# Performance work log

Measured on AMD Instinct MI355X. Metric: run time of the kernel, lower is better.

Reference implementation:

```python
import jax, jax.numpy as jnp
import numpy as np

N_NODES = 50000


def setup_inputs() -> dict:
    key = jax.random.key(0)
    k1, k2, k3, k4 = jax.random.split(key, 4)
    x = jax.random.normal(k1, (N_NODES, 128), dtype=jnp.float32)
    edge_index = jax.random.randint(k2, (2, 800000), 0, N_NODES, dtype=jnp.int64)
    W = jax.random.normal(k3, (128, 128), dtype=jnp.float32) * 0.05
    b = jax.random.normal(k4, (128,), dtype=jnp.float32) * 0.05
    return {"x": x, "edge_index": edge_index, "W": W, "b": b}


def reference(x, edge_index, W, b):
    # x: [N, C_in], edge_index: [2, E]
    row, col = edge_index[0], edge_index[1]
    n = x.shape[0]
    # degree of each node as a source (bincount over row)
    deg = jax.ops.segment_sum(jnp.ones_like(row, dtype=x.dtype), row, num_segments=n)
    # deg^{-1/2} with inf -> 0 (deg == 0 case)
    deg_inv_sqrt = jnp.where(deg > 0, jax.lax.rsqrt(jnp.maximum(deg, 1.0)) * jnp.where(deg > 0, 1.0, 0.0), 0.0)
    deg_inv_sqrt = jnp.where(deg > 0, deg ** -0.5, 0.0)
    norm = deg_inv_sqrt[row] * deg_inv_sqrt[col]  # [E]
    # gather, scale, scatter-add: agg[row] += x[col] * norm
    msgs = x[col] * norm[:, None]  # [E, C_in]
    agg = jax.ops.segment_sum(msgs, row, num_segments=n)  # [N, C_in]
    # linear
    return agg @ W.T + b
```

## Files before the change

kernel.cpp:

```cpp
#include <hip/hip_runtime.h>
#include <hip/hip_bf16.h>


typedef short v8s __attribute__((ext_vector_type(8)));
typedef float v4f __attribute__((ext_vector_type(4)));

#define ELLCAP 64
#define NSHARD 16
#define SUBCAP 384
#define ROWSTRIDE 136

static __device__ __forceinline__ unsigned int f2bf(float f) {
    __hip_bfloat16 h = __float2bfloat16(f);
    return (unsigned int)__builtin_bit_cast(unsigned short, h);
}

__global__ __launch_bounds__(256) void k_bin(
    const int* __restrict__ idx, int* __restrict__ gbin,
    unsigned int* __restrict__ pairs, const float4* __restrict__ w4,
    ushort4* __restrict__ wb4, const float2* __restrict__ x2,
    unsigned int* __restrict__ xs32, int E, int ncast, int N, int nbins) {
    int b = blockIdx.x;
    const int t = threadIdx.x;
    if (b < 16) {
        int i = b * 256 + t;
        float4 v = w4[i];
        ushort4 o;
        o.x = (unsigned short)f2bf(v.x);
        o.y = (unsigned short)f2bf(v.y);
        o.z = (unsigned short)f2bf(v.z);
        o.w = (unsigned short)f2bf(v.w);
        wb4[i] = o;
        return;
    }
    b -= 16;
    if (b < ncast) {
        int base = b * 4096;
#pragma unroll 4
        for (int it = 0; it < 16; ++it) {
            int i = base + it * 256 + t;
            int lr = i >> 6;
            unsigned ov = 0u;
            if (lr < N) {
                float2 v = x2[i];
                ov = f2bf(v.x) | (f2bf(v.y) << 16);
            }
            xs32[i] = ov;
        }
        return;
    }
    b -= ncast;
    __shared__ int hist[256];
    __shared__ int hist2[256];
    __shared__ int base[256];
    hist[t] = 0;
    hist2[t] = 0;
    __syncthreads();

    int e0 = b * 2048 + t * 8;
    int nv = E - e0;
    nv = nv > 8 ? 8 : (nv < 0 ? 0 : nv);
    int rows[8], cols[8];
    if (nv == 8) {
        int4 a0 = *(const int4*)&idx[e0];
        int4 a1 = *(const int4*)&idx[e0 + 4];
        int4 c0 = *(const int4*)&idx[E + e0];
        int4 c1 = *(const int4*)&idx[E + e0 + 4];
        rows[0] = a0.x; rows[1] = a0.y; rows[2] = a0.z; rows[3] = a0.w;
        rows[4] = a1.x; rows[5] = a1.y; rows[6] = a1.z; rows[7] = a1.w;
        cols[0] = c0.x; cols[1] = c0.y; cols[2] = c0.z; cols[3] = c0.w;
        cols[4] = c1.x; cols[5] = c1.y; cols[6] = c1.z; cols[7] = c1.w;
    } else {
        for (int k = 0; k < 8; ++k) {
            rows[k] = (k < nv) ? idx[e0 + k] : 0;
            cols[k] = (k < nv) ? idx[E + e0 + k] : 0;
        }
    }
#pragma unroll
    for (int k = 0; k < 8; ++k)
        if (k < nv) atomicAdd(&hist[rows[k] >> 8], 1);
    __syncthreads();
    const int shard = b & (NSHARD - 1);
    if (t < nbins)
        base[t] = atomicAdd(&gbin[t * NSHARD + shard], hist[t]);
    __syncthreads();
#pragma unroll
    for (int k = 0; k < 8; ++k) {
        if (k < nv) {
            int bin = rows[k] >> 8;
            int pos = base[bin] + atomicAdd(&hist2[bin], 1);
            if (pos < SUBCAP)
                pairs[((size_t)bin * NSHARD + shard) * SUBCAP + pos] =
                    (unsigned)(((rows[k] & 255) << 16) | cols[k]);
        }
    }
}

__global__ __launch_bounds__(1024) void k_deg(
    const unsigned int* __restrict__ pairs, const int* __restrict__ gbin,
    float* __restrict__ dis, int N) {
    __shared__ int cnt[256];
    __shared__ int scnt[NSHARD];
    const int bin = blockIdx.x;
    const int t = threadIdx.x;
    if (t < 256) cnt[t] = 0;
    if (t < NSHARD) {
        int m = gbin[bin * NSHARD + t];
        scnt[t] = m > SUBCAP ? SUBCAP : m;
    }
    __syncthreads();
    for (int s = 0; s < NSHARD; ++s) {
        int ms = scnt[s];
        size_t pb = ((size_t)bin * NSHARD + s) * SUBCAP;
        for (int i = t; i < ms; i += 1024)
            atomicAdd(&cnt[pairs[pb + i] >> 16], 1);
    }
    __syncthreads();
    if (t < 256) {
        int r = bin * 256 + t;
        int d = cnt[t];
        dis[r] = (r < N && d > 0) ? rsqrtf((float)d) : 0.f;
    }
}

__global__ __launch_bounds__(512) void k_fused(
    const unsigned int* __restrict__ pairs, const int* __restrict__ gbin,
    const float* __restrict__ dis, const unsigned int* __restrict__ xs32,
    const v8s* __restrict__ Wb8, const float* __restrict__ bias,
    float* __restrict__ out, int N) {
    __shared__ __align__(16) unsigned short lell[64 * ELLCAP];
    __shared__ int cnt[64];
    __shared__ int scnt[NSHARD];
    __shared__ __align__(16) unsigned short smem[64 * ROWSTRIDE];
    const int bin = blockIdx.x >> 2, sub = blockIdx.x & 3;
    const int t = threadIdx.x;
    if (t < 64) cnt[t] = 0;
    if (t < NSHARD) {
        int m = gbin[bin * NSHARD + t];
        scnt[t] = m > SUBCAP ? SUBCAP : m;
    }
    __syncthreads();
    for (int s = 0; s < NSHARD; ++s) {
        int ms = scnt[s];
        size_t pb = ((size_t)bin * NSHARD + s) * SUBCAP;
        for (int i = t; i < ms; i += 512) {
            unsigned pv = pairs[pb + i];
            int lr = pv >> 16;
            if ((lr >> 6) == sub) {
                int slot = atomicAdd(&cnt[lr & 63], 1);
                if (slot < ELLCAP)
                    lell[(lr & 63) * ELLCAP + slot] = (unsigned short)(pv & 0xFFFF);
            }
        }
    }
    __syncthreads();

    const int wv = t >> 6, lane = t & 63;
    const int r0 = bin * 256 + sub * 64;
    for (int i = 0; i < 8; ++i) {
        int lrow = wv * 8 + i;
        int n = r0 + lrow;
        float acc0 = 0.f, acc1 = 0.f;
        if (n < N) {
            int dtrue = cnt[lrow];
            int d = dtrue > ELLCAP ? ELLCAP : dtrue;
            int cl = lell[lrow * ELLCAP + lane];
            int c = (lane < d) ? cl : N;
            float dcf = dis[c];
            int dcb = __builtin_bit_cast(int, dcf);
            for (int j = 0; j < d; j += 16) {
                int cc[16];
#pragma unroll
                for (int u = 0; u < 16; ++u)
                    cc[u] = __builtin_amdgcn_readlane(c, j + u);
                unsigned uu[16];
#pragma unroll
                for (int u = 0; u < 16; ++u)
                    uu[u] = xs32[(size_t)cc[u] * 64 + lane];
                float sc[16];
#pragma unroll
                for (int u = 0; u < 16; ++u)
                    sc[u] = __builtin_bit_cast(
                        float, __builtin_amdgcn_readlane(dcb, j + u));
#pragma unroll
                for (int u = 0; u < 16; ++u) {
                    acc0 = fmaf(sc[u], __builtin_bit_cast(float, uu[u] << 16), acc0);
                    acc1 = fmaf(sc[u],
                                __builtin_bit_cast(float, uu[u] & 0xFFFF0000u), acc1);
                }
            }
            float s = (dtrue > 0) ? rsqrtf((float)dtrue) : 0.f;
            acc0 *= s;
            acc1 *= s;
        }
        unsigned pack = f2bf(acc0) | (f2bf(acc1) << 16);
        *(unsigned int*)&smem[(size_t)lrow * ROWSTRIDE + lane * 2] = pack;
    }
    __syncthreads();

    {
        int g = wv >> 2, w4 = wv & 3;
        int quad = lane >> 4, m16 = lane & 15;
        int lrow = g * 32 + (w4 & 1) * 16 + m16;
        v8s afrag[4];
#pragma unroll
        for (int kk = 0; kk < 4; ++kk)
            afrag[kk] = *(const v8s*)&smem[lrow * ROWSTRIDE + kk * 32 + quad * 8];
        int rbase = r0 + g * 32 + (w4 & 1) * 16 + quad * 4;
        int jbase = (w4 >> 1) * 64;
#pragma unroll
        for (int jt = 0; jt < 4; ++jt) {
            int jcol = jbase + jt * 16 + m16;
            v4f acc = {0.f, 0.f, 0.f, 0.f};
#pragma unroll
            for (int kk = 0; kk < 4; ++kk) {
                v8s bfrag = Wb8[jcol * 16 + kk * 4 + quad];
                acc = __builtin_amdgcn_mfma_f32_16x16x32_bf16(afrag[kk], bfrag,
                                                              acc, 0, 0, 0);
            }
            float bj = bias[jcol];
#pragma unroll
            for (int r = 0; r < 4; ++r) {
                int row = rbase + r;
                if (row < N) out[(size_t)row * 128 + jcol] = acc[r] + bj;
            }
        }
    }
}

extern "C" void kernel_launch(void* const* d_in, const int* in_sizes, int n_in,
                              void* d_out, int out_size, void* d_ws, size_t ws_size,
                              hipStream_t stream) {
    const float* x = (const float*)d_in[0];
    const int* idx = (const int*)d_in[1];
    const float* W = (const float*)d_in[2];
    const float* b = (const float*)d_in[3];
    float* out = (float*)d_out;

    const int N = in_sizes[0] / 128;
    const int E = in_sizes[1] / 2;
    const int nbins = (N + 255) / 256;
    const int nrows = nbins * 256;
    const int ncast = nbins * 4;

    char* p = (char*)d_ws;
    auto alloc = [&](size_t bytes) {
        char* r = p;
        p += (bytes + 63) & ~(size_t)63;
        return r;
    };
    int* gbin = (int*)alloc((size_t)nbins * NSHARD * 4);
    unsigned int* pairs =
        (unsigned int*)alloc((size_t)nbins * NSHARD * SUBCAP * 4);
    float* dis = (float*)alloc((size_t)nrows * 4);
    unsigned int* xs = (unsigned int*)alloc((size_t)nrows * 128 * 2);
    ushort4* wb = (ushort4*)alloc(128 * 128 * 2);

    hipMemsetAsync(gbin, 0, (size_t)nbins * NSHARD * sizeof(int), stream);

    const int bblocks = 16 + ncast + (E + 2047) / 2048;
    k_bin<<<bblocks, 256, 0, stream>>>(idx, gbin, pairs, (const float4*)W, wb,
                                       (const float2*)x, xs, E, ncast, N, nbins);
    k_deg<<<nbins, 1024, 0, stream>>>(pairs, gbin, dis, N);
    k_fused<<<nbins * 4, 512, 0, stream>>>(pairs, gbin, dis, xs, (const v8s*)wb,
                                           b, out, N);
}
```

Before: 158.7 us.

## Count degrees with global atomics in binning, shrink fused grid to 128-row blocks

Degree counting moves into the binning kernel as global atomics on a per-node counter array. The shared-memory k_deg pass is replaced by a trivial elementwise rsqrt kernel. The fused kernel now handles 128 rows per block instead of 64, cutting redundant rescans of each bin's pair list from four to two, and it gathers 32 neighbours per unrolled batch. The trade-offs are 800k global atomics in k_bin, roughly double the LDS per block (lower occupancy), and higher register pressure from the wider gather.

```diff
diff --git a/kernel.cpp b/kernel.cpp
--- a/kernel.cpp
+++ b/kernel.cpp
@@ -16,7 +16,7 @@
 }
 
 __global__ __launch_bounds__(256) void k_bin(
-    const int* __restrict__ idx, int* __restrict__ gbin,
+    const int* __restrict__ idx, int* __restrict__ gbin, int* __restrict__ deg,
     unsigned int* __restrict__ pairs, const float4* __restrict__ w4,
     ushort4* __restrict__ wb4, const float2* __restrict__ x2,
     unsigned int* __restrict__ xs32, int E, int ncast, int N, int nbins) {
@@ -77,8 +77,12 @@
         }
     }
 #pragma unroll
-    for (int k = 0; k < 8; ++k)
-        if (k < nv) atomicAdd(&hist[rows[k] >> 8], 1);
+    for (int k = 0; k < 8; ++k) {
+        if (k < nv) {
+            atomicAdd(&hist[rows[k] >> 8], 1);
+            atomicAdd(&deg[rows[k]], 1);
+        }
+    }
     __syncthreads();
     const int shard = b & (NSHARD - 1);
     if (t < nbins)
@@ -96,31 +100,17 @@
     }
 }
 
-__global__ __launch_bounds__(1024) void k_deg(
-    const unsigned int* __restrict__ pairs, const int* __restrict__ gbin,
-    float* __restrict__ dis, int N) {
-    __shared__ int cnt[256];
-    __shared__ int scnt[NSHARD];
-    const int bin = blockIdx.x;
-    const int t = threadIdx.x;
-    if (t < 256) cnt[t] = 0;
-    if (t < NSHARD) {
-        int m = gbin[bin * NSHARD + t];
-        scnt[t] = m > SUBCAP ? SUBCAP : m;
-    }
-    __syncthreads();
-    for (int s = 0; s < NSHARD; ++s) {
-        int ms = scnt[s];
-        size_t pb = ((size_t)bin * NSHARD + s) * SUBCAP;
-        for (int i = t; i < ms; i += 1024)
-            atomicAdd(&cnt[pairs[pb + i] >> 16], 1);
-    }
-    __syncthreads();
-    if (t < 256) {
-        int r = bin * 256 + t;
-        int d = cnt[t];
-        dis[r] = (r < N && d > 0) ? rsqrtf((float)d) : 0.f;
-    }
+__global__ __launch_bounds__(256) void k_dis(const int* __restrict__ deg,
+                                             float* __restrict__ dis, int N,
+                                             int nrows) {
+    int r = blockIdx.x * 256 + threadIdx.x;
+    if (r >= nrows) return;
+    float v = 0.f;
+    if (r < N) {
+        int d = deg[r];
+        if (d > 0) v = rsqrtf((float)d);
+    }
+    dis[r] = v;
 }
 
 __global__ __launch_bounds__(512) void k_fused(
@@ -128,13 +118,13 @@
     const float* __restrict__ dis, const unsigned int* __restrict__ xs32,
     const v8s* __restrict__ Wb8, const float* __restrict__ bias,
     float* __restrict__ out, int N) {
-    __shared__ __align__(16) unsigned short lell[64 * ELLCAP];
-    __shared__ int cnt[64];
+    __shared__ __align__(16) unsigned short lell[128 * ELLCAP];
+    __shared__ int cnt[128];
     __shared__ int scnt[NSHARD];
-    __shared__ __align__(16) unsigned short smem[64 * ROWSTRIDE];
-    const int bin = blockIdx.x >> 2, sub = blockIdx.x & 3;
+    __shared__ __align__(16) unsigned short smem[128 * ROWSTRIDE];
+    const int bin = blockIdx.x >> 1, sub = blockIdx.x & 1;
     const int t = threadIdx.x;
-    if (t < 64) cnt[t] = 0;
+    if (t < 128) cnt[t] = 0;
     if (t < NSHARD) {
         int m = gbin[bin * NSHARD + t];
         scnt[t] = m > SUBCAP ? SUBCAP : m;
@@ -146,19 +136,20 @@
         for (int i = t; i < ms; i += 512) {
             unsigned pv = pairs[pb + i];
             int lr = pv >> 16;
-            if ((lr >> 6) == sub) {
-                int slot = atomicAdd(&cnt[lr & 63], 1);
+            if ((lr >> 7) == sub) {
+                int la = lr & 127;
+                int slot = atomicAdd(&cnt[la], 1);
                 if (slot < ELLCAP)
-                    lell[(lr & 63) * ELLCAP + slot] = (unsigned short)(pv & 0xFFFF);
+                    lell[la * ELLCAP + slot] = (unsigned short)(pv & 0xFFFF);
             }
         }
     }
     __syncthreads();
 
     const int wv = t >> 6, lane = t & 63;
-    const int r0 = bin * 256 + sub * 64;
-    for (int i = 0; i < 8; ++i) {
-        int lrow = wv * 8 + i;
+    const int r0 = bin * 256 + sub * 128;
+    for (int i = 0; i < 16; ++i) {
+        int lrow = wv * 16 + i;
         int n = r0 + lrow;
         float acc0 = 0.f, acc1 = 0.f;
         if (n < N) {
@@ -168,28 +159,28 @@
             int c = (lane < d) ? cl : N;
             float dcf = dis[c];
             int dcb = __builtin_bit_cast(int, dcf);
-            for (int j = 0; j < d; j += 16) {
-                int cc[16];
-#pragma unroll
-                for (int u = 0; u < 16; ++u)
+            for (int j = 0; j < d; j += 32) {
+                int cc[32];
+#pragma unroll
+                for (int u = 0; u < 32; ++u)
                     cc[u] = __builtin_amdgcn_readlane(c, j + u);
-                unsigned uu[16];
-#pragma unroll
-                for (int u = 0; u < 16; ++u)
+                unsigned uu[32];
+#pragma unroll
+                for (int u = 0; u < 32; ++u)
                     uu[u] = xs32[(size_t)cc[u] * 64 + lane];
-                float sc[16];
-#pragma unroll
-                for (int u = 0; u < 16; ++u)
+                float sc[32];
+#pragma unroll
+                for (int u = 0; u < 32; ++u)
                     sc[u] = __builtin_bit_cast(
                         float, __builtin_amdgcn_readlane(dcb, j + u));
 #pragma unroll
-                for (int u = 0; u < 16; ++u) {
+                for (int u = 0; u < 32; ++u) {
                     acc0 = fmaf(sc[u], __builtin_bit_cast(float, uu[u] << 16), acc0);
                     acc1 = fmaf(sc[u],
                                 __builtin_bit_cast(float, uu[u] & 0xFFFF0000u), acc1);
                 }
             }
-            float s = (dtrue > 0) ? rsqrtf((float)dtrue) : 0.f;
+            float s = dis[n];
             acc0 *= s;
             acc1 *= s;
         }
@@ -201,28 +192,31 @@
     {
         int g = wv >> 2, w4 = wv & 3;
         int quad = lane >> 4, m16 = lane & 15;
-        int lrow = g * 32 + (w4 & 1) * 16 + m16;
-        v8s afrag[4];
-#pragma unroll
-        for (int kk = 0; kk < 4; ++kk)
-            afrag[kk] = *(const v8s*)&smem[lrow * ROWSTRIDE + kk * 32 + quad * 8];
-        int rbase = r0 + g * 32 + (w4 & 1) * 16 + quad * 4;
-        int jbase = (w4 >> 1) * 64;
-#pragma unroll
-        for (int jt = 0; jt < 4; ++jt) {
-            int jcol = jbase + jt * 16 + m16;
-            v4f acc = {0.f, 0.f, 0.f, 0.f};
-#pragma unroll
-            for (int kk = 0; kk < 4; ++kk) {
-                v8s bfrag = Wb8[jcol * 16 + kk * 4 + quad];
-                acc = __builtin_amdgcn_mfma_f32_16x16x32_bf16(afrag[kk], bfrag,
-                                                              acc, 0, 0, 0);
-            }
-            float bj = bias[jcol];
-#pragma unroll
-            for (int r = 0; r < 4; ++r) {
-                int row = rbase + r;
-                if (row < N) out[(size_t)row * 128 + jcol] = acc[r] + bj;
+#pragma unroll
+        for (int rg = 0; rg < 2; ++rg) {
+            int lrow = rg * 64 + g * 32 + (w4 & 1) * 16 + m16;
+            v8s afrag[4];
+#pragma unroll
+            for (int kk = 0; kk < 4; ++kk)
+                afrag[kk] = *(const v8s*)&smem[lrow * ROWSTRIDE + kk * 32 + quad * 8];
+            int rbase = r0 + rg * 64 + g * 32 + (w4 & 1) * 16 + quad * 4;
+            int jbase = (w4 >> 1) * 64;
+#pragma unroll
+            for (int jt = 0; jt < 4; ++jt) {
+                int jcol = jbase + jt * 16 + m16;
+                v4f acc = {0.f, 0.f, 0.f, 0.f};
+#pragma unroll
+                for (int kk = 0; kk < 4; ++kk) {
+                    v8s bfrag = Wb8[jcol * 16 + kk * 4 + quad];
+                    acc = __builtin_amdgcn_mfma_f32_16x16x32_bf16(afrag[kk], bfrag,
+                                                                  acc, 0, 0, 0);
+                }
+                float bj = bias[jcol];
+#pragma unroll
+                for (int r = 0; r < 4; ++r) {
+                    int row = rbase + r;
+                    if (row < N) out[(size_t)row * 128 + jcol] = acc[r] + bj;
+                }
             }
         }
     }
@@ -249,19 +243,21 @@
         p += (bytes + 63) & ~(size_t)63;
         return r;
     };
-    int* gbin = (int*)alloc((size_t)nbins * NSHARD * 4);
+    int* deg = (int*)alloc((size_t)nrows * 4 + (size_t)nbins * NSHARD * 4);
+    int* gbin = deg + nrows;
     unsigned int* pairs =
         (unsigned int*)alloc((size_t)nbins * NSHARD * SUBCAP * 4);
     float* dis = (float*)alloc((size_t)nrows * 4);
     unsigned int* xs = (unsigned int*)alloc((size_t)nrows * 128 * 2);
     ushort4* wb = (ushort4*)alloc(128 * 128 * 2);
 
-    hipMemsetAsync(gbin, 0, (size_t)nbins * NSHARD * sizeof(int), stream);
+    hipMemsetAsync(deg, 0, ((size_t)nrows + (size_t)nbins * NSHARD) * 4, stream);
 
     const int bblocks = 16 + ncast + (E + 2047) / 2048;
-    k_bin<<<bblocks, 256, 0, stream>>>(idx, gbin, pairs, (const float4*)W, wb,
-                                       (const float2*)x, xs, E, ncast, N, nbins);
-    k_deg<<<nbins, 1024, 0, stream>>>(pairs, gbin, dis, N);
-    k_fused<<<nbins * 4, 512, 0, stream>>>(pairs, gbin, dis, xs, (const v8s*)wb,
+    k_bin<<<bblocks, 256, 0, stream>>>(idx, gbin, deg, pairs, (const float4*)W,
+                                       wb, (const float2*)x, xs, E, ncast, N,
+                                       nbins);
+    k_dis<<<nrows / 256, 256, 0, stream>>>(deg, dis, N, nrows);
+    k_fused<<<nbins * 2, 512, 0, stream>>>(pairs, gbin, dis, xs, (const v8s*)wb,
                                            b, out, N);
 }
```

After: 187.5 us. +18.1%, slower.
